# Kernel tuning notes

Hardware: AMD Instinct MI355X
Metric: run time of the kernel (lower is better)

The kernel has to match this reference:

```python
import jax, jax.numpy as jnp
import numpy as np

T, B, IN, H, F, OUT = 2048, 32, 256, 512, 2048, 256


def setup_inputs() -> dict:
    key = jax.random.key(0)
    ks = jax.random.split(key, 9)
    s_in = 1.0 / np.sqrt(IN)
    s_h = 1.0 / np.sqrt(H)
    s_f = 1.0 / np.sqrt(F)
    return {
        "x": jax.random.normal(ks[0], (T, B, IN), dtype=jnp.float32),
        "Wg": jax.random.uniform(ks[1], (H, IN), jnp.float32, -s_in, s_in),
        "bg": jax.random.uniform(ks[2], (H,), jnp.float32, -s_in, s_in),
        "Wi": jax.random.uniform(ks[3], (H, IN), jnp.float32, -s_in, s_in),
        "bi": jax.random.uniform(ks[4], (H,), jnp.float32, -s_in, s_in),
        "W1": jax.random.uniform(ks[5], (F, H), jnp.float32, -s_h, s_h),
        "b1": jax.random.uniform(ks[6], (F,), jnp.float32, -s_h, s_h),
        "W2": jax.random.uniform(ks[7], (OUT, F), jnp.float32, -s_f, s_f),
        "b2": jax.random.uniform(ks[8], (OUT,), jnp.float32, -s_f, s_f),
    }


def _gilr_scan(a, b):
    # h_t = a_t * h_{t-1} + b_t with h_0 = 0  ->  parallel associative scan over time
    def combine(c1, c2):
        a1, b1 = c1
        a2, b2 = c2
        return (a1 * a2, b1 * a2 + b2)
    _, h = jax.lax.associative_scan(combine, (a, b), axis=0)
    return h


def reference(x, Wg, bg, Wi, bi, W1, b1, W2, b2):
    # x: (T, B, IN)
    g = jax.nn.sigmoid(jnp.einsum("tbi,hi->tbh", x, Wg) + bg)  # (T,B,H)
    i = jnp.tanh(jnp.einsum("tbi,hi->tbh", x, Wi) + bi)        # (T,B,H)
    h = _gilr_scan(g, (1.0 - g) * i)                             # (T,B,H)
    z = jax.nn.gelu(jnp.einsum("tbh,fh->tbf", h, W1) + b1, approximate=False)
    out = jnp.einsum("tbf,of->tbo", z, W2) + b2                  # (T,B,OUT)
    return out
```

## Files before the change

kernel.cpp:

```cpp
#include <hip/hip_runtime.h>
#include <hip/hip_fp16.h>
#include <math.h>


#define IN_DIM 256
#define H_DIM 512
#define F_DIM 2048
#define OUT_DIM 256

typedef _Float16 f16;
typedef _Float16 f16x8 __attribute__((ext_vector_type(8)));
typedef float f32x4 __attribute__((ext_vector_type(4)));

#define AS3(p) ((__attribute__((address_space(3))) void*)(p))
#define AS1(p) ((const __attribute__((address_space(1))) void*)(p))
#define MFMA16(d, x, y) d = __builtin_amdgcn_mfma_f32_16x16x32_f16(x, y, d, 0, 0, 0)


__global__ void cvt_kernel(const float* __restrict__ in, f16* __restrict__ out, int n8) {
  int i = blockIdx.x * blockDim.x + threadIdx.x;
  if (i >= n8) return;
  const float4* p = (const float4*)in + (size_t)i * 2;
  float4 a = p[0], b = p[1];
  f16x8 o = { (f16)a.x, (f16)a.y, (f16)a.z, (f16)a.w,
              (f16)b.x, (f16)b.y, (f16)b.z, (f16)b.w };
  *((f16x8*)out + i) = o;
}

__global__ void cvt_w(const float* __restrict__ Wg, const float* __restrict__ Wi,
                      const float* __restrict__ W1, const float* __restrict__ W2,
                      f16* __restrict__ wgi, f16* __restrict__ w1, f16* __restrict__ w2) {
  int i = blockIdx.x * 256 + threadIdx.x;
  const float* src; f16* dst; int l;
  if (i < 16384)       { l = i;          src = Wg + (size_t)l * 8; dst = wgi + (size_t)l * 8; }
  else if (i < 32768)  { l = i - 16384;  src = Wi + (size_t)l * 8; dst = wgi + 131072 + (size_t)l * 8; }
  else if (i < 163840) { l = i - 32768;  src = W1 + (size_t)l * 8; dst = w1 + (size_t)l * 8; }
  else                 { l = i - 163840; src = W2 + (size_t)l * 8; dst = w2 + (size_t)l * 8; }
  float4 a = ((const float4*)src)[0], b = ((const float4*)src)[1];
  f16x8 o = { (f16)a.x, (f16)a.y, (f16)a.z, (f16)a.w,
              (f16)b.x, (f16)b.y, (f16)b.z, (f16)b.w };
  *(f16x8*)dst = o;
}

__global__ void bias_cat_kernel(const float* __restrict__ bg, const float* __restrict__ bi,
                                float* __restrict__ bgi) {
  int t = threadIdx.x;
  bgi[t] = (t < 512) ? bg[t] : bi[t - 512];
}

__device__ __forceinline__ float sigmoid_fast(float v) {
  return __builtin_amdgcn_rcpf(1.0f + __expf(-v));
}
__device__ __forceinline__ float tanh_fast(float v) {
  return 1.0f - 2.0f * __builtin_amdgcn_rcpf(__expf(2.0f * v) + 1.0f);
}
__device__ __forceinline__ float gelu_fast(float v) {
  float u = v * v;
  float y = v * fmaf(0.0713548353f, u, 1.59576912161f);
  return v * __builtin_amdgcn_rcpf(1.0f + __expf(-y));
}


__global__ __launch_bounds__(256, 4) void gemm1_t2(
    const f16* __restrict__ A, const f16* __restrict__ Bw,
    const float* __restrict__ bias, f16* __restrict__ Cout) {
  constexpr int LDA = 256, LDB = 256, LDC = 1024, NT = 8;
  __shared__ f16 lds[2][2][128][32];
  const int tid = threadIdx.x, wid = tid >> 6, lane = tid & 63;
  const int bid = blockIdx.x;
  const int m0 = ((bid & 7) * 32 + (bid >> 6)) * 128;
  const int n0 = ((bid >> 3) & 7) * 128;
  const int wr = (wid >> 1) * 64, wc = (wid & 1) * 64;

  const f16* srcA[2]; const f16* srcB[2];
#pragma unroll
  for (int q = 0; q < 2; ++q) {
    int s = (wid * 2 + q) * 64 + lane;
    int row = s >> 2, g = (s & 3) ^ ((row >> 1) & 3);
    srcA[q] = A + (size_t)(m0 + row) * LDA + g * 8;
    srcB[q] = Bw + (size_t)(n0 + row) * LDB + g * 8;
  }
  auto stage = [&](int buf, int kt) {
    f16* la = &lds[buf][0][0][0] + (wid * 2) * 512;
    f16* lb = &lds[buf][1][0][0] + (wid * 2) * 512;
#pragma unroll
    for (int q = 0; q < 2; ++q) {
      __builtin_amdgcn_global_load_lds(AS1(srcA[q] + kt * 32), AS3(la + q * 512), 16, 0, 0);
      __builtin_amdgcn_global_load_lds(AS1(srcB[q] + kt * 32), AS3(lb + q * 512), 16, 0, 0);
    }
  };
  const int r = lane & 15;
  const int cs = (((lane >> 4) ^ ((lane >> 1) & 3)) << 3);

  f32x4 acc[4][4] = {};
  stage(0, 0);
  for (int kt = 0; kt < NT; ++kt) {
    __syncthreads();
    if (kt + 1 < NT) stage((kt + 1) & 1, kt + 1);
    f16(*At)[32] = lds[kt & 1][0];
    f16(*Bt)[32] = lds[kt & 1][1];
    f16x8 af[4], bf[4];
#pragma unroll
    for (int i = 0; i < 4; ++i) af[i] = *(const f16x8*)&At[wr + i * 16 + r][cs];
#pragma unroll
    for (int i = 0; i < 4; ++i) bf[i] = *(const f16x8*)&Bt[wc + i * 16 + r][cs];
#pragma unroll
    for (int mi = 0; mi < 4; ++mi)
#pragma unroll
      for (int ni = 0; ni < 4; ++ni)
        MFMA16(acc[mi][ni], af[mi], bf[ni]);
  }

  __syncthreads();
  const bool sig = n0 < 512;
  f16* ep = &lds[0][0][0][0] + wid * 4096;
  const int rq = (lane >> 4) * 4;
#pragma unroll
  for (int ni = 0; ni < 4; ++ni) {
    float bv = bias[n0 + wc + ni * 16 + r];
    int cc = ni * 2 + (r >> 3);
#pragma unroll
    for (int mi = 0; mi < 4; ++mi) {
#pragma unroll
      for (int j = 0; j < 4; ++j) {
        int lrow = mi * 16 + rq + j;
        float v = acc[mi][ni][j] + bv;
        float av = sig ? sigmoid_fast(v) : tanh_fast(v);
        ep[lrow * 64 + ((cc ^ (lrow & 7)) << 3) + (r & 7)] = (f16)av;
      }
    }
  }
  asm volatile("s_waitcnt lgkmcnt(0)" ::: "memory");
  __builtin_amdgcn_sched_barrier(0);
#pragma unroll
  for (int t = 0; t < 8; ++t) {
    int idx = t * 64 + lane;
    int row = idx >> 3, c = idx & 7;
    f16x8 v = *(const f16x8*)(ep + row * 64 + ((c ^ (row & 7)) << 3));
    *(f16x8*)(Cout + (size_t)(m0 + wr + row) * LDC + n0 + wc + c * 8) = v;
  }
}


__global__ __launch_bounds__(256, 3) void gemm1_t3(
    const f16* __restrict__ A, const f16* __restrict__ Bw,
    const float* __restrict__ bias, f16* __restrict__ Cout) {
  constexpr int LDA = 256, LDB = 256, LDC = 1024, NT = 8;
  __shared__ f16 lds[3][2][128][32];
  const int tid = threadIdx.x, wid = tid >> 6, lane = tid & 63;
  const int bid = blockIdx.x;
  const int m0 = ((bid & 7) * 32 + (bid >> 6)) * 128;
  const int n0 = ((bid >> 3) & 7) * 128;
  const int wr = (wid >> 1) * 64, wc = (wid & 1) * 64;

  const f16* srcA[2]; const f16* srcB[2];
#pragma unroll
  for (int q = 0; q < 2; ++q) {
    int s = (wid * 2 + q) * 64 + lane;
    int row = s >> 2, g = (s & 3) ^ ((row >> 1) & 3);
    srcA[q] = A + (size_t)(m0 + row) * LDA + g * 8;
    srcB[q] = Bw + (size_t)(n0 + row) * LDB + g * 8;
  }
  auto stage = [&](int buf, int kt) {
    f16* la = &lds[buf][0][0][0] + (wid * 2) * 512;
    f16* lb = &lds[buf][1][0][0] + (wid * 2) * 512;
#pragma unroll
    for (int q = 0; q < 2; ++q) {
      __builtin_amdgcn_global_load_lds(AS1(srcA[q] + kt * 32), AS3(la + q * 512), 16, 0, 0);
      __builtin_amdgcn_global_load_lds(AS1(srcB[q] + kt * 32), AS3(lb + q * 512), 16, 0, 0);
    }
  };
  const int r = lane & 15;
  const int cs = (((lane >> 4) ^ ((lane >> 1) & 3)) << 3);

  f32x4 acc[4][4] = {};
  stage(0, 0); stage(1, 1);
  asm volatile("s_waitcnt vmcnt(4)" ::: "memory");
  __syncthreads();
#pragma unroll
  for (int kt = 0; kt < NT; ++kt) {
    if (kt + 2 < NT) stage((kt + 2) % 3, kt + 2);
    f16(*At)[32] = lds[kt % 3][0];
    f16(*Bt)[32] = lds[kt % 3][1];
    f16x8 af[4], bf[4];
#pragma unroll
    for (int i = 0; i < 4; ++i) af[i] = *(const f16x8*)&At[wr + i * 16 + r][cs];
#pragma unroll
    for (int i = 0; i < 4; ++i) bf[i] = *(const f16x8*)&Bt[wc + i * 16 + r][cs];
#pragma unroll
    for (int mi = 0; mi < 4; ++mi)
#pragma unroll
      for (int ni = 0; ni < 4; ++ni)
        MFMA16(acc[mi][ni], af[mi], bf[ni]);
    if (kt + 1 < NT) {
      if (kt + 2 < NT) asm volatile("s_waitcnt vmcnt(4)" ::: "memory");
      else             asm volatile("s_waitcnt vmcnt(0)" ::: "memory");
      __syncthreads();
    }
  }

  __syncthreads();
  const bool sig = n0 < 512;
  f16* ep = &lds[0][0][0][0] + wid * 4096;
  const int rq = (lane >> 4) * 4;
#pragma unroll
  for (int ni = 0; ni < 4; ++ni) {
    float bv = bias[n0 + wc + ni * 16 + r];
    int cc = ni * 2 + (r >> 3);
#pragma unroll
    for (int mi = 0; mi < 4; ++mi) {
#pragma unroll
      for (int j = 0; j < 4; ++j) {
        int lrow = mi * 16 + rq + j;
        float v = acc[mi][ni][j] + bv;
        float av = sig ? sigmoid_fast(v) : tanh_fast(v);
        ep[lrow * 64 + ((cc ^ (lrow & 7)) << 3) + (r & 7)] = (f16)av;
      }
    }
  }
  asm volatile("s_waitcnt lgkmcnt(0)" ::: "memory");
  __builtin_amdgcn_sched_barrier(0);
#pragma unroll
  for (int t = 0; t < 8; ++t) {
    int idx = t * 64 + lane;
    int row = idx >> 3, c = idx & 7;
    f16x8 v = *(const f16x8*)(ep + row * 64 + ((c ^ (row & 7)) << 3));
    *(f16x8*)(Cout + (size_t)(m0 + wr + row) * LDC + n0 + wc + c * 8) = v;
  }
}


__global__ __launch_bounds__(256, 2) void gemm2_k(
    const f16* __restrict__ A, const f16* __restrict__ Bw,
    const float* __restrict__ bias, f16* __restrict__ Cout, int mpb) {
  constexpr int LDA = 1024, LDB = 512, LDC = 2048, NT = 16;
  __shared__ f16 lds[24576];
  const int tid = threadIdx.x, wid = tid >> 6, lane = tid & 63;
  const int lr = lane & 15;
  const int bid = blockIdx.x;
  const int m0 = ((bid & 7) * mpb + (bid >> 7)) * 256;
  const int n0 = ((bid >> 3) & 15) * 128;
  const int wr = (wid >> 1) * 128, wc = (wid & 1) * 64;

  const f16* srcA[4];
  const f16* srcB[2];
#pragma unroll
  for (int q = 0; q < 4; ++q) {
    int s = wid * 256 + q * 64 + lane;
    int row = s >> 2, g = (s & 3) ^ ((row >> 1) & 3);
    srcA[q] = A + (size_t)(m0 + row) * LDA + g * 8;
  }
#pragma unroll
  for (int q = 0; q < 2; ++q) {
    int s = wid * 128 + q * 64 + lane;
    int row = s >> 2, g = (s & 3) ^ ((row >> 1) & 3);
    srcB[q] = Bw + (size_t)(n0 + row) * LDB + g * 8;
  }
  auto stage = [&](int buf, int kt) {
#pragma unroll
    for (int q = 0; q < 4; ++q)
      __builtin_amdgcn_global_load_lds(AS1(srcA[q] + kt * 32),
          AS3(lds + buf * 8192 + wid * 2048 + q * 512), 16, 0, 0);
#pragma unroll
    for (int q = 0; q < 2; ++q)
      __builtin_amdgcn_global_load_lds(AS1(srcB[q] + kt * 32),
          AS3(lds + 16384 + buf * 4096 + wid * 1024 + q * 512), 16, 0, 0);
  };

  const int qsf = (((lane >> 4) ^ ((lr >> 1) & 3)) << 3);
  f32x4 acc[8][4] = {};
  stage(0, 0);
  for (int kt = 0; kt < NT; ++kt) {
    const int cur = kt & 1;
    __syncthreads();
    if (kt + 1 < NT) stage(cur ^ 1, kt + 1);
    f16x8 af[8], bf[4];
#pragma unroll
    for (int mi = 0; mi < 8; ++mi)
      af[mi] = *(const f16x8*)(lds + cur * 8192 + (wr + mi * 16 + lr) * 32 + qsf);
#pragma unroll
    for (int ni = 0; ni < 4; ++ni)
      bf[ni] = *(const f16x8*)(lds + 16384 + cur * 4096 + (wc + ni * 16 + lr) * 32 + qsf);
#pragma unroll
    for (int mi = 0; mi < 8; ++mi)
#pragma unroll
      for (int ni = 0; ni < 4; ++ni)
        MFMA16(acc[mi][ni], af[mi], bf[ni]);
  }

  __syncthreads();
  f16* ep = lds + wid * 4096;
  const int rq = (lane >> 4) * 4;
#pragma unroll
  for (int h = 0; h < 2; ++h) {
#pragma unroll
    for (int mi = 0; mi < 4; ++mi) {
#pragma unroll
      for (int ni = 0; ni < 4; ++ni) {
        float bv = bias[n0 + wc + ni * 16 + lr];
        int cc = ni * 2 + (lr >> 3);
#pragma unroll
        for (int j = 0; j < 4; ++j) {
          int lrow = mi * 16 + rq + j;
          float v = gelu_fast(acc[h * 4 + mi][ni][j] + bv);
          ep[lrow * 64 + ((cc ^ (lrow & 7)) << 3) + (lr & 7)] = (f16)v;
        }
      }
    }
    asm volatile("s_waitcnt lgkmcnt(0)" ::: "memory");
    __builtin_amdgcn_sched_barrier(0);
#pragma unroll
    for (int t = 0; t < 8; ++t) {
      int idx = t * 64 + lane;
      int row = idx >> 3, c = idx & 7;
      f16x8 v = *(const f16x8*)(ep + row * 64 + ((c ^ (row & 7)) << 3));
      *(f16x8*)(Cout + (size_t)(m0 + wr + h * 64 + row) * LDC + n0 + wc + c * 8) = v;
    }
    asm volatile("s_waitcnt lgkmcnt(0)" ::: "memory");
    __builtin_amdgcn_sched_barrier(0);
  }
}


__global__ __launch_bounds__(256, 2) void gemm3_k(
    const f16* __restrict__ A, const f16* __restrict__ Bw,
    const float* __restrict__ bias, float* __restrict__ Cout, int mpx) {
  constexpr int LDA = 2048, LDB = 2048, LDC = 256, NT = 32;
  __shared__ f16 lds[2][2][128][64];
  const int tid = threadIdx.x, wid = tid >> 6, lane = tid & 63;
  const int bid = blockIdx.x;
  const int m0 = ((bid & 7) * mpx + (bid >> 4)) * 128;
  const int n0 = ((bid >> 3) & 1) * 128;
  const int wr = (wid >> 1) * 64, wc = (wid & 1) * 64;

  auto stage = [&](int buf, int kt) {
    const f16* ga = A + (size_t)m0 * LDA + kt * 64;
    const f16* gb = Bw + (size_t)n0 * LDB + kt * 64;
    f16* la = &lds[buf][0][0][0];
    f16* lb = &lds[buf][1][0][0];
#pragma unroll
    for (int q = 0; q < 4; ++q) {
      int seg = (wid << 2) + q;
      int s = seg * 64 + lane;
      int row = s >> 3, col = (s & 7) << 3;
      __builtin_amdgcn_global_load_lds(AS1(ga + (size_t)row * LDA + col),
                                       AS3(la + seg * 512), 16, 0, 0);
      __builtin_amdgcn_global_load_lds(AS1(gb + (size_t)row * LDB + col),
                                       AS3(lb + seg * 512), 16, 0, 0);
    }
  };

  f32x4 acc[4][4] = {};
  stage(0, 0);
  for (int kt = 0; kt < NT; ++kt) {
    __syncthreads();
    if (kt + 1 < NT) stage((kt + 1) & 1, kt + 1);
    f16(*At)[64] = lds[kt & 1][0];
    f16(*Bt)[64] = lds[kt & 1][1];
    const int r = lane & 15, cg = (lane >> 4) << 3;
#pragma unroll
    for (int kk = 0; kk < 2; ++kk) {
      f16x8 af[4], bf[4];
#pragma unroll
      for (int i = 0; i < 4; ++i)
        af[i] = *(const f16x8*)&At[wr + i * 16 + r][kk * 32 + cg];
#pragma unroll
      for (int i = 0; i < 4; ++i)
        bf[i] = *(const f16x8*)&Bt[wc + i * 16 + r][kk * 32 + cg];
#pragma unroll
      for (int mi = 0; mi < 4; ++mi)
#pragma unroll
        for (int ni = 0; ni < 4; ++ni)
          MFMA16(acc[mi][ni], af[mi], bf[ni]);
    }
  }
  const int r = lane & 15, rq = (lane >> 4) * 4;
#pragma unroll
  for (int ni = 0; ni < 4; ++ni) {
    int col = n0 + wc + ni * 16 + r;
    float bv = bias[col];
#pragma unroll
    for (int mi = 0; mi < 4; ++mi) {
#pragma unroll
      for (int j = 0; j < 4; ++j) {
        int row = m0 + wr + mi * 16 + rq + j;
        Cout[(size_t)row * LDC + col] = acc[mi][ni][j] + bv;
      }
    }
  }
}


#define NCH 16384
#define NCHUNK 32
#define CLEN 64

__global__ void scan_p1(const f16* __restrict__ ab, float* __restrict__ cA,
                        float* __restrict__ cH) {
  int ch = blockIdx.x * 256 + threadIdx.x;
  int c = blockIdx.y;
  const f16* pg = ab + (size_t)(c * CLEN) * 32768 + (ch >> 9) * 1024 + (ch & 511);
  const f16* pi = pg + 512;
  float A = 1.f, Hl = 0.f;
  for (int t = 0; t < CLEN; ++t) {
    float g = (float)pg[0];
    float ii = (float)pi[0];
    Hl = fmaf(g, Hl - ii, ii);
    A *= g;
    pg += 32768; pi += 32768;
  }
  cA[c * NCH + ch] = A;
  cH[c * NCH + ch] = Hl;
}

__global__ void scan_p2(const float* __restrict__ cA, const float* __restrict__ cH,
                        float* __restrict__ st) {
  int ch = blockIdx.x * 256 + threadIdx.x;
  float h0 = 0.f;
  for (int c = 0; c < NCHUNK; ++c) {
    st[c * NCH + ch] = h0;
    h0 = cA[c * NCH + ch] * h0 + cH[c * NCH + ch];
  }
}

__global__ void scan_p3(f16* __restrict__ ab, const float* __restrict__ st) {
  int ch = blockIdx.x * 256 + threadIdx.x;
  int c = blockIdx.y;
  f16* pg = ab + (size_t)(c * CLEN) * 32768 + (ch >> 9) * 1024 + (ch & 511);
  const f16* pi = pg + 512;
  float hv = st[c * NCH + ch];
  for (int t = 0; t < CLEN; ++t) {
    float g = (float)pg[0];
    float ii = (float)pi[0];
    hv = fmaf(g, hv - ii, ii);
    pg[0] = (f16)hv;
    pg += 32768; pi += 32768;
  }
}


extern "C" void kernel_launch(void* const* d_in, const int* in_sizes, int n_in,
                              void* d_out, int out_size, void* d_ws, size_t ws_size,
                              hipStream_t stream) {
  const float* x  = (const float*)d_in[0];
  const float* Wg = (const float*)d_in[1];
  const float* bg = (const float*)d_in[2];
  const float* Wi = (const float*)d_in[3];
  const float* bi = (const float*)d_in[4];
  const float* W1 = (const float*)d_in[5];
  const float* b1 = (const float*)d_in[6];
  const float* W2 = (const float*)d_in[7];
  const float* b2 = (const float*)d_in[8];
  float* out = (float*)d_out;

  char* ws = (char*)d_ws;
  f16*   wgi16 = (f16*)(ws + 0);
  f16*   w116  = (f16*)(ws + 524288);
  f16*   w216  = (f16*)(ws + 2621440);
  float* bgi   = (float*)(ws + 3670016);
  f16*   x16   = (f16*)(ws + 4194304);
  f16*   ab16  = (f16*)(ws + 37748736);
  float* cA    = (float*)(ws + 171966464);
  float* cH    = (float*)(ws + 174063616);
  float* st    = (float*)(ws + 176160768);
  f16*   z16   = (f16*)(ws + 178257920);
  if (ws_size < 245366784) return;

  cvt_w<<<896, 256, 0, stream>>>(Wg, Wi, W1, W2, wgi16, w116, w216);
  bias_cat_kernel<<<1, 1024, 0, stream>>>(bg, bi, bgi);
  cvt_kernel<<<8192, 256, 0, stream>>>(x, x16, 2097152);

  gemm1_t2<<<2048, 256, 0, stream>>>(x16, wgi16, bgi, ab16);
  gemm1_t3<<<2048, 256, 0, stream>>>(x16 + (size_t)32768 * 256, wgi16, bgi,
                                     ab16 + (size_t)32768 * 1024);

  scan_p1<<<dim3(64, NCHUNK), 256, 0, stream>>>(ab16, cA, cH);
  scan_p2<<<64, 256, 0, stream>>>(cA, cH, st);
  scan_p3<<<dim3(64, NCHUNK), 256, 0, stream>>>(ab16, st);

  const int nslab = (ws_size >= 312475648ULL) ? 2 : 4;
  const int rows  = 65536 / nslab;
  const int mpb   = 32 / nslab;
  const int mpx   = 64 / nslab;
  for (int s = 0; s < nslab; ++s) {
    const f16* hs = ab16 + (size_t)s * rows * 1024;
    gemm2_k<<<128 * mpb, 256, 0, stream>>>(hs, w116, b1, z16, mpb);
    gemm3_k<<<16 * mpx, 256, 0, stream>>>(z16, w216, b2,
                                          out + (size_t)s * rows * 256, mpx);
  }
}
```

Measured before the change: 482.6 us.

## Fix 4-slab GEMM schedule, raise gemm2 occupancy, add narrow-N gemm3 variant

The FFN stage now always runs in four slabs with hardcoded tile mappings, where before it picked two or four slabs depending on workspace size. gemm2 asks for three blocks per SM through launch_bounds. A new gemm3_h kernel with 128x64 tiles and 512 blocks handles the last two slabs, while gemm3_k with 256 blocks still handles the first two. The aim is better occupancy and more blocks in flight for the small output GEMM, at the cost of possible register spills in gemm2 and more slab launches when the two-slab path would have been usable.

```diff
diff --git a/kernel.cpp b/kernel.cpp
--- a/kernel.cpp
+++ b/kernel.cpp
@@ -230,15 +230,15 @@
 }
 
 
-__global__ __launch_bounds__(256, 2) void gemm2_k(
+__global__ __launch_bounds__(256, 3) void gemm2_k3(
     const f16* __restrict__ A, const f16* __restrict__ Bw,
-    const float* __restrict__ bias, f16* __restrict__ Cout, int mpb) {
+    const float* __restrict__ bias, f16* __restrict__ Cout) {
   constexpr int LDA = 1024, LDB = 512, LDC = 2048, NT = 16;
   __shared__ f16 lds[24576];
   const int tid = threadIdx.x, wid = tid >> 6, lane = tid & 63;
   const int lr = lane & 15;
   const int bid = blockIdx.x;
-  const int m0 = ((bid & 7) * mpb + (bid >> 7)) * 256;
+  const int m0 = ((bid & 7) * 8 + (bid >> 7)) * 256;
   const int n0 = ((bid >> 3) & 15) * 128;
   const int wr = (wid >> 1) * 128, wc = (wid & 1) * 64;
 
@@ -324,12 +324,12 @@
 
 __global__ __launch_bounds__(256, 2) void gemm3_k(
     const f16* __restrict__ A, const f16* __restrict__ Bw,
-    const float* __restrict__ bias, float* __restrict__ Cout, int mpx) {
+    const float* __restrict__ bias, float* __restrict__ Cout) {
   constexpr int LDA = 2048, LDB = 2048, LDC = 256, NT = 32;
   __shared__ f16 lds[2][2][128][64];
   const int tid = threadIdx.x, wid = tid >> 6, lane = tid & 63;
   const int bid = blockIdx.x;
-  const int m0 = ((bid & 7) * mpx + (bid >> 4)) * 128;
+  const int m0 = ((bid & 7) * 16 + (bid >> 4)) * 128;
   const int n0 = ((bid >> 3) & 1) * 128;
   const int wr = (wid >> 1) * 64, wc = (wid & 1) * 64;
 
@@ -377,6 +377,79 @@
   const int r = lane & 15, rq = (lane >> 4) * 4;
 #pragma unroll
   for (int ni = 0; ni < 4; ++ni) {
+    int col = n0 + wc + ni * 16 + r;
+    float bv = bias[col];
+#pragma unroll
+    for (int mi = 0; mi < 4; ++mi) {
+#pragma unroll
+      for (int j = 0; j < 4; ++j) {
+        int row = m0 + wr + mi * 16 + rq + j;
+        Cout[(size_t)row * LDC + col] = acc[mi][ni][j] + bv;
+      }
+    }
+  }
+}
+
+
+__global__ __launch_bounds__(256, 2) void gemm3_h(
+    const f16* __restrict__ A, const f16* __restrict__ Bw,
+    const float* __restrict__ bias, float* __restrict__ Cout) {
+  constexpr int LDA = 2048, LDB = 2048, LDC = 256, NT = 32;
+  __shared__ f16 lds[24576];
+  const int tid = threadIdx.x, wid = tid >> 6, lane = tid & 63;
+  const int bid = blockIdx.x;
+  const int m0 = ((bid & 7) * 16 + (bid >> 5)) * 128;
+  const int n0 = ((bid >> 3) & 3) * 64;
+  const int wr = (wid >> 1) * 64, wc = (wid & 1) * 32;
+
+  auto stage = [&](int buf, int kt) {
+    const f16* ga = A + (size_t)m0 * LDA + kt * 64;
+    const f16* gb = Bw + (size_t)n0 * LDB + kt * 64;
+#pragma unroll
+    for (int q = 0; q < 4; ++q) {
+      int seg = wid * 4 + q;
+      int s = seg * 64 + lane;
+      int row = s >> 3, col = (s & 7) << 3;
+      __builtin_amdgcn_global_load_lds(AS1(ga + (size_t)row * LDA + col),
+                                       AS3(lds + buf * 8192 + seg * 512), 16, 0, 0);
+    }
+#pragma unroll
+    for (int q = 0; q < 2; ++q) {
+      int seg = wid * 2 + q;
+      int s = seg * 64 + lane;
+      int row = s >> 3, col = (s & 7) << 3;
+      __builtin_amdgcn_global_load_lds(AS1(gb + (size_t)row * LDB + col),
+                                       AS3(lds + 16384 + buf * 4096 + seg * 512), 16, 0, 0);
+    }
+  };
+
+  f32x4 acc[4][2] = {};
+  stage(0, 0);
+  for (int kt = 0; kt < NT; ++kt) {
+    __syncthreads();
+    if (kt + 1 < NT) stage((kt + 1) & 1, kt + 1);
+    const f16* At = lds + (kt & 1) * 8192;
+    const f16* Bt = lds + 16384 + (kt & 1) * 4096;
+    const int r = lane & 15, cg = (lane >> 4) << 3;
+#pragma unroll
+    for (int kk = 0; kk < 2; ++kk) {
+      f16x8 af[4], bf[2];
+#pragma unroll
+      for (int i = 0; i < 4; ++i)
+        af[i] = *(const f16x8*)(At + (wr + i * 16 + r) * 64 + kk * 32 + cg);
+#pragma unroll
+      for (int i = 0; i < 2; ++i)
+        bf[i] = *(const f16x8*)(Bt + (wc + i * 16 + r) * 64 + kk * 32 + cg);
+#pragma unroll
+      for (int mi = 0; mi < 4; ++mi)
+#pragma unroll
+        for (int ni = 0; ni < 2; ++ni)
+          MFMA16(acc[mi][ni], af[mi], bf[ni]);
+    }
+  }
+  const int r = lane & 15, rq = (lane >> 4) * 4;
+#pragma unroll
+  for (int ni = 0; ni < 2; ++ni) {
     int col = n0 + wc + ni * 16 + r;
     float bv = bias[col];
 #pragma unroll
@@ -478,14 +551,12 @@
   scan_p2<<<64, 256, 0, stream>>>(cA, cH, st);
   scan_p3<<<dim3(64, NCHUNK), 256, 0, stream>>>(ab16, st);
 
-  const int nslab = (ws_size >= 312475648ULL) ? 2 : 4;
-  const int rows  = 65536 / nslab;
-  const int mpb   = 32 / nslab;
-  const int mpx   = 64 / nslab;
-  for (int s = 0; s < nslab; ++s) {
-    const f16* hs = ab16 + (size_t)s * rows * 1024;
-    gemm2_k<<<128 * mpb, 256, 0, stream>>>(hs, w116, b1, z16, mpb);
-    gemm3_k<<<16 * mpx, 256, 0, stream>>>(z16, w216, b2,
-                                          out + (size_t)s * rows * 256, mpx);
-  }
-}
+  for (int s = 0; s < 4; ++s) {
+    const f16* hs = ab16 + (size_t)s * 16384 * 1024;
+    gemm2_k3<<<1024, 256, 0, stream>>>(hs, w116, b1, z16);
+    if (s < 2)
+      gemm3_k<<<256, 256, 0, stream>>>(z16, w216, b2, out + (size_t)s * 16384 * 256);
+    else
+      gemm3_h<<<512, 256, 0, stream>>>(z16, w216, b2, out + (size_t)s * 16384 * 256);
+  }
+}
```

New measurement: 476.2 us. No clear change (-1.3%).

## Fix four slabs and shrink gemm3 tile to 128x64 for more blocks

Applied to the files above, without the earlier changes.

Hardcodes four slabs of 16384 rows for the h->z->out GEMM chain, so each z slab stays smaller and more likely cache-resident. gemm2 raises its launch-bounds occupancy hint from 2 to 3 blocks per CU. gemm3 halves its N tile from 128 to 64, doubling its grid to 512 blocks to fill more CUs, at the cost of re-reading A tiles twice as often. Forcing 3 blocks per CU may cause register spills in gemm2.

```diff
diff --git a/kernel.cpp b/kernel.cpp
--- a/kernel.cpp
+++ b/kernel.cpp
@@ -230,15 +230,15 @@
 }
 
 
-__global__ __launch_bounds__(256, 2) void gemm2_k(
+__global__ __launch_bounds__(256, 3) void gemm2_a(
     const f16* __restrict__ A, const f16* __restrict__ Bw,
-    const float* __restrict__ bias, f16* __restrict__ Cout, int mpb) {
+    const float* __restrict__ bias, f16* __restrict__ Cout) {
   constexpr int LDA = 1024, LDB = 512, LDC = 2048, NT = 16;
   __shared__ f16 lds[24576];
   const int tid = threadIdx.x, wid = tid >> 6, lane = tid & 63;
   const int lr = lane & 15;
   const int bid = blockIdx.x;
-  const int m0 = ((bid & 7) * mpb + (bid >> 7)) * 256;
+  const int m0 = ((bid & 7) * 8 + (bid >> 7)) * 256;
   const int n0 = ((bid >> 3) & 15) * 128;
   const int wr = (wid >> 1) * 128, wc = (wid & 1) * 64;
 
@@ -322,61 +322,65 @@
 }
 
 
-__global__ __launch_bounds__(256, 2) void gemm3_k(
+__global__ __launch_bounds__(256, 2) void gemm3_h(
     const f16* __restrict__ A, const f16* __restrict__ Bw,
-    const float* __restrict__ bias, float* __restrict__ Cout, int mpx) {
+    const float* __restrict__ bias, float* __restrict__ Cout) {
   constexpr int LDA = 2048, LDB = 2048, LDC = 256, NT = 32;
-  __shared__ f16 lds[2][2][128][64];
+  __shared__ f16 lds[24576];
   const int tid = threadIdx.x, wid = tid >> 6, lane = tid & 63;
   const int bid = blockIdx.x;
-  const int m0 = ((bid & 7) * mpx + (bid >> 4)) * 128;
-  const int n0 = ((bid >> 3) & 1) * 128;
-  const int wr = (wid >> 1) * 64, wc = (wid & 1) * 64;
+  const int m0 = ((bid & 7) * 16 + (bid >> 5)) * 128;
+  const int n0 = ((bid >> 3) & 3) * 64;
+  const int wr = (wid >> 1) * 64, wc = (wid & 1) * 32;
 
   auto stage = [&](int buf, int kt) {
     const f16* ga = A + (size_t)m0 * LDA + kt * 64;
     const f16* gb = Bw + (size_t)n0 * LDB + kt * 64;
-    f16* la = &lds[buf][0][0][0];
-    f16* lb = &lds[buf][1][0][0];
 #pragma unroll
     for (int q = 0; q < 4; ++q) {
-      int seg = (wid << 2) + q;
+      int seg = wid * 4 + q;
       int s = seg * 64 + lane;
       int row = s >> 3, col = (s & 7) << 3;
       __builtin_amdgcn_global_load_lds(AS1(ga + (size_t)row * LDA + col),
-                                       AS3(la + seg * 512), 16, 0, 0);
+                                       AS3(lds + buf * 8192 + seg * 512), 16, 0, 0);
+    }
+#pragma unroll
+    for (int q = 0; q < 2; ++q) {
+      int seg = wid * 2 + q;
+      int s = seg * 64 + lane;
+      int row = s >> 3, col = (s & 7) << 3;
       __builtin_amdgcn_global_load_lds(AS1(gb + (size_t)row * LDB + col),
-                                       AS3(lb + seg * 512), 16, 0, 0);
+                                       AS3(lds + 16384 + buf * 4096 + seg * 512), 16, 0, 0);
     }
   };
 
-  f32x4 acc[4][4] = {};
+  f32x4 acc[4][2] = {};
   stage(0, 0);
   for (int kt = 0; kt < NT; ++kt) {
     __syncthreads();
     if (kt + 1 < NT) stage((kt + 1) & 1, kt + 1);
-    f16(*At)[64] = lds[kt & 1][0];
-    f16(*Bt)[64] = lds[kt & 1][1];
+    const f16* At = lds + (kt & 1) * 8192;
+    const f16* Bt = lds + 16384 + (kt & 1) * 4096;
     const int r = lane & 15, cg = (lane >> 4) << 3;
 #pragma unroll
     for (int kk = 0; kk < 2; ++kk) {
-      f16x8 af[4], bf[4];
+      f16x8 af[4], bf[2];
 #pragma unroll
       for (int i = 0; i < 4; ++i)
-        af[i] = *(const f16x8*)&At[wr + i * 16 + r][kk * 32 + cg];
-#pragma unroll
-      for (int i = 0; i < 4; ++i)
-        bf[i] = *(const f16x8*)&Bt[wc + i * 16 + r][kk * 32 + cg];
+        af[i] = *(const f16x8*)(At + (wr + i * 16 + r) * 64 + kk * 32 + cg);
+#pragma unroll
+      for (int i = 0; i < 2; ++i)
+        bf[i] = *(const f16x8*)(Bt + (wc + i * 16 + r) * 64 + kk * 32 + cg);
 #pragma unroll
       for (int mi = 0; mi < 4; ++mi)
 #pragma unroll
-        for (int ni = 0; ni < 4; ++ni)
+        for (int ni = 0; ni < 2; ++ni)
           MFMA16(acc[mi][ni], af[mi], bf[ni]);
     }
   }
   const int r = lane & 15, rq = (lane >> 4) * 4;
 #pragma unroll
-  for (int ni = 0; ni < 4; ++ni) {
+  for (int ni = 0; ni < 2; ++ni) {
     int col = n0 + wc + ni * 16 + r;
     float bv = bias[col];
 #pragma unroll
@@ -478,14 +482,9 @@
   scan_p2<<<64, 256, 0, stream>>>(cA, cH, st);
   scan_p3<<<dim3(64, NCHUNK), 256, 0, stream>>>(ab16, st);
 
-  const int nslab = (ws_size >= 312475648ULL) ? 2 : 4;
-  const int rows  = 65536 / nslab;
-  const int mpb   = 32 / nslab;
-  const int mpx   = 64 / nslab;
-  for (int s = 0; s < nslab; ++s) {
-    const f16* hs = ab16 + (size_t)s * rows * 1024;
-    gemm2_k<<<128 * mpb, 256, 0, stream>>>(hs, w116, b1, z16, mpb);
-    gemm3_k<<<16 * mpx, 256, 0, stream>>>(z16, w216, b2,
-                                          out + (size_t)s * rows * 256, mpx);
-  }
-}
+  for (int s = 0; s < 4; ++s) {
+    const f16* hs = ab16 + (size_t)s * 16384 * 1024;
+    gemm2_a<<<1024, 256, 0, stream>>>(hs, w116, b1, z16);
+    gemm3_h<<<512, 256, 0, stream>>>(z16, w216, b2, out + (size_t)s * 16384 * 256);
+  }
+}
```

New measurement: 474.4 us (median of 2 runs). Within noise of the previous version (-1.7%).
